# Optimization experiments

Measured on AMD Instinct MI355X. Metric: run time of the kernel, lower is better.

## Reference

```python
import jax, jax.numpy as jnp
import numpy as np

B, IN, P, H, OUT = 131072, 40, 128, 256, 1

def setup_inputs() -> dict:
    key = jax.random.key(0)
    ks = jax.random.split(key, 10)
    s_in, s_h = 1.0 / np.sqrt(IN), 1.0 / np.sqrt(H)
    return {
        "x_step": jax.random.normal(ks[0], (B, 1, IN), jnp.float32),
        "hidden_in": jax.random.normal(ks[1], (1, B, H), jnp.float32),
        "W_proj": jax.random.uniform(ks[2], (P, IN), jnp.float32, -s_in, s_in),
        "b_proj": jax.random.uniform(ks[3], (P,), jnp.float32, -s_in, s_in),
        "W_ih": jax.random.uniform(ks[4], (3 * H, P), jnp.float32, -s_h, s_h),
        "W_hh": jax.random.uniform(ks[5], (3 * H, H), jnp.float32, -s_h, s_h),
        "b_ih": jax.random.uniform(ks[6], (3 * H,), jnp.float32, -s_h, s_h),
        "b_hh": jax.random.uniform(ks[7], (3 * H,), jnp.float32, -s_h, s_h),
        "W_head": jax.random.uniform(ks[8], (OUT, H), jnp.float32, -s_h, s_h),
        "b_head": jax.random.uniform(ks[9], (OUT,), jnp.float32, -s_h, s_h),
    }

def reference(x_step, hidden_in, W_proj, b_proj, W_ih, W_hh, b_ih, b_hh, W_head, b_head):
    # input projection: [B,1,IN] -> [B,P]
    x = jnp.einsum('bi,pi->bp', x_step[:, 0, :], W_proj) + b_proj
    h = hidden_in[0]  # [B,H]
    # single GRU step (PyTorch gate layout: reset, update, new)
    gi = jnp.einsum('bp,gp->bg', x, W_ih) + b_ih  # [B,3H]
    gh = jnp.einsum('bh,gh->bg', h, W_hh) + b_hh  # [B,3H]
    i_r, i_z, i_n = jnp.split(gi, 3, axis=-1)
    h_r, h_z, h_n = jnp.split(gh, 3, axis=-1)
    r = jax.nn.sigmoid(i_r + h_r)
    z = jax.nn.sigmoid(i_z + h_z)
    n = jnp.tanh(i_n + r * h_n)
    h_new = (1.0 - z) * n + z * h  # [B,H]
    pred = jnp.einsum('bh,oh->bo', h_new, W_head) + b_head  # [B,OUT]
    return pred[:, None, :], h_new[None]  # ([B,1,OUT], [1,B,H])
```

## Files before the change

### kernel.cpp

```cpp
#include <hip/hip_runtime.h>

#define B_N 131072
#define IN_N 40
#define H_N 256

typedef __bf16 bf16x8 __attribute__((ext_vector_type(8)));
typedef float f32x4 __attribute__((ext_vector_type(4)));

#define MFMA(a, b, c) __builtin_amdgcn_mfma_f32_16x16x32_bf16(a, b, c, 0, 0, 0)

#define WSQ 61440
#define WSBI (4 * WSQ)
#define PREP_N (245760 + 768 + B_N)

__global__ void prep(const float* __restrict__ Wp, const float* __restrict__ bp,
                     const float* __restrict__ Wih, const float* __restrict__ Whh,
                     const float* __restrict__ bih, const float* __restrict__ bhead,
                     __bf16* __restrict__ wsb, float* __restrict__ out) {
  int i = blockIdx.x * 256 + threadIdx.x;
  if (i < WSBI) {
    const int quarter = i / WSQ, r = i % WSQ;
    if (r < 49152) {
      const int g = r >> 14, ks = (r >> 11) & 7, sub = (r >> 9) & 3,
                col = (r >> 3) & 63, e = r & 7;
      const int gatecol = g * 256 + quarter * 64 + col;
      const int k = ks * 32 + sub * 8 + e;
      wsb[i] = (__bf16)Whh[(size_t)gatecol * 256 + k];
    } else {
      const int rr = r - 49152;
      const int g = rr >> 12, ks = (rr >> 11) & 1, sub = (rr >> 9) & 3,
                col = (rr >> 3) & 63, e = rr & 7;
      const int gatecol = g * 256 + quarter * 64 + col;
      const int k = ks * 32 + sub * 8 + e;
      float v = 0.f;
      if (k < IN_N)
        for (int p = 0; p < 128; ++p)
          v += Wih[(size_t)gatecol * 128 + p] * Wp[p * IN_N + k];
      wsb[i] = (__bf16)v;
    }
  } else if (i < WSBI + 768) {
    const int g = i - WSBI;
    float v = bih[g];
    for (int p = 0; p < 128; ++p) v += Wih[g * 128 + p] * bp[p];
    ((float*)(wsb + WSBI))[g] = v;
  } else if (i < PREP_N) {
    out[i - (WSBI + 768)] = bhead[0];
  }
}

__device__ __forceinline__ void gload16(const __bf16* g, __bf16* l) {
  __builtin_amdgcn_global_load_lds(
      (const __attribute__((address_space(1))) void*)g,
      (__attribute__((address_space(3))) void*)l, 16, 0, 0);
}

__device__ __forceinline__ bf16x8 cvt8(float4 a, float4 b) {
  bf16x8 u;
  u[0] = (__bf16)a.x; u[1] = (__bf16)a.y; u[2] = (__bf16)a.z; u[3] = (__bf16)a.w;
  u[4] = (__bf16)b.x; u[5] = (__bf16)b.y; u[6] = (__bf16)b.z; u[7] = (__bf16)b.w;
  return u;
}

__global__ __launch_bounds__(512, 1) void gru_v13(
    const float* __restrict__ x, const float* __restrict__ h0,
    const __bf16* __restrict__ wsb, const float* __restrict__ bhh,
    const float* __restrict__ Whead, float* __restrict__ out) {
  __shared__ __bf16 Wl[WSQ];
  __shared__ __bf16 hsw[16384];
  __shared__ __bf16 xsw[4096];

  const int tid = threadIdx.x;
  const int lane = tid & 63;
  const int w = tid >> 6;
  const int l15 = lane & 15;
  const int l4 = lane >> 4;
  const int rw = w >> 2, cw = w & 3;

  const int lin = (blockIdx.x & 7) * 128 + (blockIdx.x >> 3);
  const int quarter = lin & 3;
  const int rgrp = lin >> 2;
  const size_t row0 = (size_t)rgrp * 512;

  const int colB = cw * 16 + l15;
  const int hcol = quarter * 64 + colB;

  const __bf16* wsq = wsb + quarter * WSQ;
#pragma unroll
  for (int j = 0; j < 15; ++j) {
    const int c = (w * 15 + j) * 512;
    gload16(wsq + c + lane * 8, &Wl[c]);
  }

  if (tid < 192) {
    const int row = tid / 3, cz = 5 + tid % 3;
    bf16x8 z = {};
    *reinterpret_cast<bf16x8*>(&xsw[row * 64 + ((cz ^ (row & 7)) << 3)]) = z;
  }

  const float* bfused = (const float*)(wsb + WSBI);
  const float bR = bfused[hcol] + bhh[hcol];
  const float bZ = bfused[256 + hcol] + bhh[256 + hcol];
  const float bI = bfused[512 + hcol];
  const float bH = bhh[512 + hcol];
  const float wh = Whead[hcol];

  float4 shv[8], sxv[2];
  const int xrow = tid / 5, xci = tid % 5;
  auto issueStage = [&](int t) {
    const float* hb = h0 + (row0 + (size_t)t * 64) * H_N;
#pragma unroll
    for (int j = 0; j < 4; ++j) {
      const int g = tid + j * 512;
      shv[2 * j]     = *reinterpret_cast<const float4*>(hb + g * 8);
      shv[2 * j + 1] = *reinterpret_cast<const float4*>(hb + g * 8 + 4);
    }
    if (tid < 320) {
      const float* xb = x + (row0 + (size_t)t * 64) * IN_N + xrow * IN_N + xci * 8;
      sxv[0] = *reinterpret_cast<const float4*>(xb);
      sxv[1] = *reinterpret_cast<const float4*>(xb + 4);
    }
  };
  auto writeStage = [&]() {
#pragma unroll
    for (int j = 0; j < 4; ++j) {
      const int g = tid + j * 512;
      const int row = g >> 5, ci = g & 31;
      *reinterpret_cast<bf16x8*>(&hsw[row * 256 + ((ci ^ (row & 7)) << 3)]) =
          cvt8(shv[2 * j], shv[2 * j + 1]);
    }
    if (tid < 320)
      *reinterpret_cast<bf16x8*>(&xsw[xrow * 64 + ((xci ^ (xrow & 7)) << 3)]) =
          cvt8(sxv[0], sxv[1]);
  };

  issueStage(0);
  writeStage();
  __syncthreads();

  for (int t = 0; t < 8; ++t) {
    if (t < 7) issueStage(t + 1);

    f32x4 aR[2], aZ[2], aI[2], aH[2];
#pragma unroll
    for (int mi = 0; mi < 2; ++mi) {
      aR[mi] = (f32x4){bR, bR, bR, bR};
      aZ[mi] = (f32x4){bZ, bZ, bZ, bZ};
      aI[mi] = (f32x4){bI, bI, bI, bI};
      aH[mi] = (f32x4){bH, bH, bH, bH};
    }

#pragma unroll
    for (int ks = 0; ks < 10; ++ks) {
      bf16x8 b0, b1, b2;
      if (ks < 2) {
        const int base = 49152 + l4 * 512 + colB * 8;
        b0 = *reinterpret_cast<const bf16x8*>(&Wl[base + (0 * 2 + ks) * 2048]);
        b1 = *reinterpret_cast<const bf16x8*>(&Wl[base + (1 * 2 + ks) * 2048]);
        b2 = *reinterpret_cast<const bf16x8*>(&Wl[base + (2 * 2 + ks) * 2048]);
      } else {
        const int base = l4 * 512 + colB * 8;
        b0 = *reinterpret_cast<const bf16x8*>(&Wl[base + (0 * 8 + ks - 2) * 2048]);
        b1 = *reinterpret_cast<const bf16x8*>(&Wl[base + (1 * 8 + ks - 2) * 2048]);
        b2 = *reinterpret_cast<const bf16x8*>(&Wl[base + (2 * 8 + ks - 2) * 2048]);
      }
#pragma unroll
      for (int mi = 0; mi < 2; ++mi) {
        const int row = rw * 32 + mi * 16 + l15;
        bf16x8 a;
        if (ks < 2)
          a = *reinterpret_cast<const bf16x8*>(
              &xsw[row * 64 + (((ks * 4 + l4) ^ (row & 7)) << 3)]);
        else
          a = *reinterpret_cast<const bf16x8*>(
              &hsw[row * 256 + ((((ks - 2) * 4 + l4) ^ (row & 7)) << 3)]);
        aR[mi] = MFMA(a, b0, aR[mi]);
        aZ[mi] = MFMA(a, b1, aZ[mi]);
        if (ks < 2) aI[mi] = MFMA(a, b2, aI[mi]);
        else        aH[mi] = MFMA(a, b2, aH[mi]);
      }
    }

    const size_t trow = row0 + (size_t)t * 64;
    const int chc = quarter * 8 + (colB >> 3), cofs = colB & 7;
    float ps[2][4];
#pragma unroll
    for (int mi = 0; mi < 2; ++mi) {
#pragma unroll
      for (int r = 0; r < 4; ++r) {
        const int rowl = rw * 32 + mi * 16 + l4 * 4 + r;
        const float rg = 1.f / (1.f + __expf(-aR[mi][r]));
        const float zg = 1.f / (1.f + __expf(-aZ[mi][r]));
        const float e2 = __expf(2.f * (aI[mi][r] + rg * aH[mi][r]));
        const float ng = (e2 - 1.f) / (e2 + 1.f);
        const float hv = (float)hsw[rowl * 256 + ((chc ^ (rowl & 7)) << 3) + cofs];
        const float hn = (1.f - zg) * ng + zg * hv;
        out[(size_t)B_N + (trow + rowl) * H_N + hcol] = hn;
        ps[mi][r] = hn * wh;
      }
    }
#pragma unroll
    for (int mi = 0; mi < 2; ++mi)
#pragma unroll
      for (int r = 0; r < 4; ++r) {
        float s = ps[mi][r];
        s += __shfl_xor(s, 1);
        s += __shfl_xor(s, 2);
        s += __shfl_xor(s, 4);
        s += __shfl_xor(s, 8);
        if (l15 == 0)
          atomicAdd(&out[trow + rw * 32 + mi * 16 + l4 * 4 + r], s);
      }

    __syncthreads();
    if (t < 7) {
      writeStage();
      __syncthreads();
    }
  }
}

extern "C" void kernel_launch(void* const* d_in, const int* in_sizes, int n_in,
                              void* d_out, int out_size, void* d_ws, size_t ws_size,
                              hipStream_t stream) {
  const float* x     = (const float*)d_in[0];
  const float* h0    = (const float*)d_in[1];
  const float* Wp    = (const float*)d_in[2];
  const float* bp    = (const float*)d_in[3];
  const float* Wih   = (const float*)d_in[4];
  const float* Whh   = (const float*)d_in[5];
  const float* bih   = (const float*)d_in[6];
  const float* bhh   = (const float*)d_in[7];
  const float* Whead = (const float*)d_in[8];
  const float* bhead = (const float*)d_in[9];
  float* out = (float*)d_out;
  __bf16* wsb = (__bf16*)d_ws;

  prep<<<(PREP_N + 255) / 256, 256, 0, stream>>>(Wp, bp, Wih, Whh, bih, bhead, wsb, out);
  gru_v13<<<1024, 512, 0, stream>>>(x, h0, wsb, bhh, Whead, out);
}
```

Baseline: 194.9 us.

## Double waves per block, shrink per-wave row tile, overlap stage write with epilogue

The workgroup grows from 512 to 1024 threads. Each of the 16 waves now computes one 16-row MFMA tile instead of two, and the staging loads and weight-to-LDS loads are spread across the larger block. The next h/x stage is written into LDS right after the MFMA loop, behind a single barrier, so one barrier per step is removed. The epilogue reads the previous hidden value from global fp32 instead of from the bf16 LDS copy. The aim is more waves to hide latency and fewer syncs, at the cost of halved B-fragment reuse per wave (more LDS reads) and extra global reads of h0.

After: 179.5 us. 1.09x faster.

```diff
diff --git a/kernel.cpp b/kernel.cpp
--- a/kernel.cpp
+++ b/kernel.cpp
@@ -61,7 +61,7 @@
   return u;
 }
 
-__global__ __launch_bounds__(512, 1) void gru_v13(
+__global__ __launch_bounds__(1024, 1) void gru_v14(
     const float* __restrict__ x, const float* __restrict__ h0,
     const __bf16* __restrict__ wsb, const float* __restrict__ bhh,
     const float* __restrict__ Whead, float* __restrict__ out) {
@@ -86,9 +86,10 @@
 
   const __bf16* wsq = wsb + quarter * WSQ;
 #pragma unroll
-  for (int j = 0; j < 15; ++j) {
-    const int c = (w * 15 + j) * 512;
-    gload16(wsq + c + lane * 8, &Wl[c]);
+  for (int j = 0; j < 8; ++j) {
+    const int idx = j * 16 + w;
+    if (idx < 120)
+      gload16(wsq + idx * 512 + lane * 8, &Wl[idx * 512]);
   }
 
   if (tid < 192) {
@@ -104,13 +105,13 @@
   const float bH = bhh[512 + hcol];
   const float wh = Whead[hcol];
 
-  float4 shv[8], sxv[2];
+  float4 shv[4], sxv[2];
   const int xrow = tid / 5, xci = tid % 5;
   auto issueStage = [&](int t) {
     const float* hb = h0 + (row0 + (size_t)t * 64) * H_N;
 #pragma unroll
-    for (int j = 0; j < 4; ++j) {
-      const int g = tid + j * 512;
+    for (int j = 0; j < 2; ++j) {
+      const int g = tid + j * 1024;
       shv[2 * j]     = *reinterpret_cast<const float4*>(hb + g * 8);
       shv[2 * j + 1] = *reinterpret_cast<const float4*>(hb + g * 8 + 4);
     }
@@ -122,8 +123,8 @@
   };
   auto writeStage = [&]() {
 #pragma unroll
-    for (int j = 0; j < 4; ++j) {
-      const int g = tid + j * 512;
+    for (int j = 0; j < 2; ++j) {
+      const int g = tid + j * 1024;
       const int row = g >> 5, ci = g & 31;
       *reinterpret_cast<bf16x8*>(&hsw[row * 256 + ((ci ^ (row & 7)) << 3)]) =
           cvt8(shv[2 * j], shv[2 * j + 1]);
@@ -140,82 +141,66 @@
   for (int t = 0; t < 8; ++t) {
     if (t < 7) issueStage(t + 1);
 
-    f32x4 aR[2], aZ[2], aI[2], aH[2];
-#pragma unroll
-    for (int mi = 0; mi < 2; ++mi) {
-      aR[mi] = (f32x4){bR, bR, bR, bR};
-      aZ[mi] = (f32x4){bZ, bZ, bZ, bZ};
-      aI[mi] = (f32x4){bI, bI, bI, bI};
-      aH[mi] = (f32x4){bH, bH, bH, bH};
-    }
-
+    f32x4 aR = {bR, bR, bR, bR};
+    f32x4 aZ = {bZ, bZ, bZ, bZ};
+    f32x4 aI = {bI, bI, bI, bI};
+    f32x4 aH = {bH, bH, bH, bH};
+
+    const int arow = rw * 16 + l15;
 #pragma unroll
     for (int ks = 0; ks < 10; ++ks) {
-      bf16x8 b0, b1, b2;
+      bf16x8 b0, b1, b2, a;
       if (ks < 2) {
         const int base = 49152 + l4 * 512 + colB * 8;
         b0 = *reinterpret_cast<const bf16x8*>(&Wl[base + (0 * 2 + ks) * 2048]);
         b1 = *reinterpret_cast<const bf16x8*>(&Wl[base + (1 * 2 + ks) * 2048]);
         b2 = *reinterpret_cast<const bf16x8*>(&Wl[base + (2 * 2 + ks) * 2048]);
+        a = *reinterpret_cast<const bf16x8*>(
+            &xsw[arow * 64 + (((ks * 4 + l4) ^ (arow & 7)) << 3)]);
       } else {
         const int base = l4 * 512 + colB * 8;
         b0 = *reinterpret_cast<const bf16x8*>(&Wl[base + (0 * 8 + ks - 2) * 2048]);
         b1 = *reinterpret_cast<const bf16x8*>(&Wl[base + (1 * 8 + ks - 2) * 2048]);
         b2 = *reinterpret_cast<const bf16x8*>(&Wl[base + (2 * 8 + ks - 2) * 2048]);
+        a = *reinterpret_cast<const bf16x8*>(
+            &hsw[arow * 256 + ((((ks - 2) * 4 + l4) ^ (arow & 7)) << 3)]);
       }
-#pragma unroll
-      for (int mi = 0; mi < 2; ++mi) {
-        const int row = rw * 32 + mi * 16 + l15;
-        bf16x8 a;
-        if (ks < 2)
-          a = *reinterpret_cast<const bf16x8*>(
-              &xsw[row * 64 + (((ks * 4 + l4) ^ (row & 7)) << 3)]);
-        else
-          a = *reinterpret_cast<const bf16x8*>(
-              &hsw[row * 256 + ((((ks - 2) * 4 + l4) ^ (row & 7)) << 3)]);
-        aR[mi] = MFMA(a, b0, aR[mi]);
-        aZ[mi] = MFMA(a, b1, aZ[mi]);
-        if (ks < 2) aI[mi] = MFMA(a, b2, aI[mi]);
-        else        aH[mi] = MFMA(a, b2, aH[mi]);
-      }
-    }
+      aR = MFMA(a, b0, aR);
+      aZ = MFMA(a, b1, aZ);
+      if (ks < 2) aI = MFMA(a, b2, aI);
+      else        aH = MFMA(a, b2, aH);
+    }
+
+    __syncthreads();
+
+    if (t < 7) writeStage();
 
     const size_t trow = row0 + (size_t)t * 64;
-    const int chc = quarter * 8 + (colB >> 3), cofs = colB & 7;
-    float ps[2][4];
-#pragma unroll
-    for (int mi = 0; mi < 2; ++mi) {
-#pragma unroll
-      for (int r = 0; r < 4; ++r) {
-        const int rowl = rw * 32 + mi * 16 + l4 * 4 + r;
-        const float rg = 1.f / (1.f + __expf(-aR[mi][r]));
-        const float zg = 1.f / (1.f + __expf(-aZ[mi][r]));
-        const float e2 = __expf(2.f * (aI[mi][r] + rg * aH[mi][r]));
-        const float ng = (e2 - 1.f) / (e2 + 1.f);
-        const float hv = (float)hsw[rowl * 256 + ((chc ^ (rowl & 7)) << 3) + cofs];
-        const float hn = (1.f - zg) * ng + zg * hv;
-        out[(size_t)B_N + (trow + rowl) * H_N + hcol] = hn;
-        ps[mi][r] = hn * wh;
-      }
-    }
-#pragma unroll
-    for (int mi = 0; mi < 2; ++mi)
-#pragma unroll
-      for (int r = 0; r < 4; ++r) {
-        float s = ps[mi][r];
-        s += __shfl_xor(s, 1);
-        s += __shfl_xor(s, 2);
-        s += __shfl_xor(s, 4);
-        s += __shfl_xor(s, 8);
-        if (l15 == 0)
-          atomicAdd(&out[trow + rw * 32 + mi * 16 + l4 * 4 + r], s);
-      }
-
-    __syncthreads();
-    if (t < 7) {
-      writeStage();
-      __syncthreads();
-    }
+    float ps[4];
+#pragma unroll
+    for (int r = 0; r < 4; ++r) {
+      const int rowl = rw * 16 + l4 * 4 + r;
+      const float rg = 1.f / (1.f + __expf(-aR[r]));
+      const float zg = 1.f / (1.f + __expf(-aZ[r]));
+      const float e2 = __expf(2.f * (aI[r] + rg * aH[r]));
+      const float ng = (e2 - 1.f) / (e2 + 1.f);
+      const float hv = h0[(trow + rowl) * H_N + hcol];
+      const float hn = (1.f - zg) * ng + zg * hv;
+      out[(size_t)B_N + (trow + rowl) * H_N + hcol] = hn;
+      ps[r] = hn * wh;
+    }
+#pragma unroll
+    for (int r = 0; r < 4; ++r) {
+      float s = ps[r];
+      s += __shfl_xor(s, 1);
+      s += __shfl_xor(s, 2);
+      s += __shfl_xor(s, 4);
+      s += __shfl_xor(s, 8);
+      if (l15 == 0)
+        atomicAdd(&out[trow + rw * 16 + l4 * 4 + r], s);
+    }
+
+    if (t < 7) __syncthreads();
   }
 }
 
@@ -236,5 +221,5 @@
   __bf16* wsb = (__bf16*)d_ws;
 
   prep<<<(PREP_N + 255) / 256, 256, 0, stream>>>(Wp, bp, Wih, Whh, bih, bhead, wsb, out);
-  gru_v13<<<1024, 512, 0, stream>>>(x, h0, wsb, bhh, Whead, out);
-}
+  gru_v14<<<1024, 1024, 0, stream>>>(x, h0, wsb, bhh, Whead, out);
+}
```

## Replace persistent 8-tile loop with one 128-row tile per 1024-thread block

Applied to the files above, without the earlier changes.

Replaces the persistent blocks, which each looped over eight 64-row tiles with register-staged prefetch, with 4096 blocks of 1024 threads that each handle one 128-row tile. The x-projection and hidden weight slices now share one LDS buffer that is reused across phases. The intent is more parallelism and less per-block serialization, with load latency hidden by many resident waves instead of explicit software pipelining. In exchange, every block reloads its weight slice into LDS (four times as many weight loads overall), extra barriers are added, and h is re-read from global memory in fp32 for the blend.

Result: slower. 271.8 us (+39.4%).

```diff
diff --git a/kernel.cpp b/kernel.cpp
--- a/kernel.cpp
+++ b/kernel.cpp
@@ -61,13 +61,12 @@
   return u;
 }
 
-__global__ __launch_bounds__(512, 1) void gru_v13(
+__global__ __launch_bounds__(1024, 1) void gru_v16(
     const float* __restrict__ x, const float* __restrict__ h0,
     const __bf16* __restrict__ wsb, const float* __restrict__ bhh,
     const float* __restrict__ Whead, float* __restrict__ out) {
-  __shared__ __bf16 Wl[WSQ];
-  __shared__ __bf16 hsw[16384];
-  __shared__ __bf16 xsw[4096];
+  __shared__ __bf16 WG[49152];
+  __shared__ __bf16 AH[32768];
 
   const int tid = threadIdx.x;
   const int lane = tid & 63;
@@ -76,25 +75,46 @@
   const int l4 = lane >> 4;
   const int rw = w >> 2, cw = w & 3;
 
-  const int lin = (blockIdx.x & 7) * 128 + (blockIdx.x >> 3);
+  const int lin = (blockIdx.x & 7) * 512 + (blockIdx.x >> 3);
   const int quarter = lin & 3;
-  const int rgrp = lin >> 2;
-  const size_t row0 = (size_t)rgrp * 512;
+  const size_t row0 = (size_t)(lin >> 2) * 128;
 
   const int colB = cw * 16 + l15;
   const int hcol = quarter * 64 + colB;
 
   const __bf16* wsq = wsb + quarter * WSQ;
 #pragma unroll
-  for (int j = 0; j < 15; ++j) {
-    const int c = (w * 15 + j) * 512;
-    gload16(wsq + c + lane * 8, &Wl[c]);
-  }
-
-  if (tid < 192) {
-    const int row = tid / 3, cz = 5 + tid % 3;
+  for (int j = 0; j < 6; ++j) {
+    const int idx = w * 6 + j;
+    gload16(wsq + idx * 512 + lane * 8, &WG[idx * 512]);
+  }
+#pragma unroll
+  for (int j = 0; j < 2; ++j) {
+    const int idx = j * 16 + w;
+    if (idx < 24)
+      gload16(wsq + 49152 + idx * 512 + lane * 8, &AH[idx * 512]);
+  }
+
+  bf16x8 hreg[4];
+#pragma unroll
+  for (int j = 0; j < 4; ++j) {
+    const int c = tid + j * 1024;
+    const float* s = h0 + (row0 + (c >> 5)) * H_N + (c & 31) * 8;
+    hreg[j] = cvt8(*reinterpret_cast<const float4*>(s),
+                   *reinterpret_cast<const float4*>(s + 4));
+  }
+
+  if (tid < 640) {
+    const int row = tid / 5, kc = tid % 5;
+    const float* s = x + (row0 + row) * IN_N + kc * 8;
+    *reinterpret_cast<bf16x8*>(&AH[12288 + row * 64 + ((kc ^ (row & 7)) << 3)]) =
+        cvt8(*reinterpret_cast<const float4*>(s),
+             *reinterpret_cast<const float4*>(s + 4));
+  } else {
+    const int p = tid - 640;
+    const int row = p / 3, kc = 5 + p % 3;
     bf16x8 z = {};
-    *reinterpret_cast<bf16x8*>(&xsw[row * 64 + ((cz ^ (row & 7)) << 3)]) = z;
+    *reinterpret_cast<bf16x8*>(&AH[12288 + row * 64 + ((kc ^ (row & 7)) << 3)]) = z;
   }
 
   const float* bfused = (const float*)(wsb + WSBI);
@@ -104,119 +124,86 @@
   const float bH = bhh[512 + hcol];
   const float wh = Whead[hcol];
 
-  float4 shv[8], sxv[2];
-  const int xrow = tid / 5, xci = tid % 5;
-  auto issueStage = [&](int t) {
-    const float* hb = h0 + (row0 + (size_t)t * 64) * H_N;
-#pragma unroll
-    for (int j = 0; j < 4; ++j) {
-      const int g = tid + j * 512;
-      shv[2 * j]     = *reinterpret_cast<const float4*>(hb + g * 8);
-      shv[2 * j + 1] = *reinterpret_cast<const float4*>(hb + g * 8 + 4);
-    }
-    if (tid < 320) {
-      const float* xb = x + (row0 + (size_t)t * 64) * IN_N + xrow * IN_N + xci * 8;
-      sxv[0] = *reinterpret_cast<const float4*>(xb);
-      sxv[1] = *reinterpret_cast<const float4*>(xb + 4);
-    }
-  };
-  auto writeStage = [&]() {
-#pragma unroll
-    for (int j = 0; j < 4; ++j) {
-      const int g = tid + j * 512;
-      const int row = g >> 5, ci = g & 31;
-      *reinterpret_cast<bf16x8*>(&hsw[row * 256 + ((ci ^ (row & 7)) << 3)]) =
-          cvt8(shv[2 * j], shv[2 * j + 1]);
-    }
-    if (tid < 320)
-      *reinterpret_cast<bf16x8*>(&xsw[xrow * 64 + ((xci ^ (xrow & 7)) << 3)]) =
-          cvt8(sxv[0], sxv[1]);
-  };
-
-  issueStage(0);
-  writeStage();
   __syncthreads();
 
-  for (int t = 0; t < 8; ++t) {
-    if (t < 7) issueStage(t + 1);
-
-    f32x4 aR[2], aZ[2], aI[2], aH[2];
+  f32x4 aR[2], aZ[2], aI[2], aH4[2];
+#pragma unroll
+  for (int mi = 0; mi < 2; ++mi) {
+    aR[mi] = (f32x4){bR, bR, bR, bR};
+    aZ[mi] = (f32x4){bZ, bZ, bZ, bZ};
+    aI[mi] = (f32x4){bI, bI, bI, bI};
+    aH4[mi] = (f32x4){bH, bH, bH, bH};
+  }
+  const int bofs = l4 * 512 + colB * 8;
+#pragma unroll
+  for (int ks = 0; ks < 2; ++ks) {
+    const bf16x8 b0 = *reinterpret_cast<const bf16x8*>(&AH[(0 + ks) * 2048 + bofs]);
+    const bf16x8 b1 = *reinterpret_cast<const bf16x8*>(&AH[(2 + ks) * 2048 + bofs]);
+    const bf16x8 b2 = *reinterpret_cast<const bf16x8*>(&AH[(4 + ks) * 2048 + bofs]);
 #pragma unroll
     for (int mi = 0; mi < 2; ++mi) {
-      aR[mi] = (f32x4){bR, bR, bR, bR};
-      aZ[mi] = (f32x4){bZ, bZ, bZ, bZ};
-      aI[mi] = (f32x4){bI, bI, bI, bI};
-      aH[mi] = (f32x4){bH, bH, bH, bH};
-    }
-
-#pragma unroll
-    for (int ks = 0; ks < 10; ++ks) {
-      bf16x8 b0, b1, b2;
-      if (ks < 2) {
-        const int base = 49152 + l4 * 512 + colB * 8;
-        b0 = *reinterpret_cast<const bf16x8*>(&Wl[base + (0 * 2 + ks) * 2048]);
-        b1 = *reinterpret_cast<const bf16x8*>(&Wl[base + (1 * 2 + ks) * 2048]);
-        b2 = *reinterpret_cast<const bf16x8*>(&Wl[base + (2 * 2 + ks) * 2048]);
-      } else {
-        const int base = l4 * 512 + colB * 8;
-        b0 = *reinterpret_cast<const bf16x8*>(&Wl[base + (0 * 8 + ks - 2) * 2048]);
-        b1 = *reinterpret_cast<const bf16x8*>(&Wl[base + (1 * 8 + ks - 2) * 2048]);
-        b2 = *reinterpret_cast<const bf16x8*>(&Wl[base + (2 * 8 + ks - 2) * 2048]);
-      }
-#pragma unroll
-      for (int mi = 0; mi < 2; ++mi) {
-        const int row = rw * 32 + mi * 16 + l15;
-        bf16x8 a;
-        if (ks < 2)
-          a = *reinterpret_cast<const bf16x8*>(
-              &xsw[row * 64 + (((ks * 4 + l4) ^ (row & 7)) << 3)]);
-        else
-          a = *reinterpret_cast<const bf16x8*>(
-              &hsw[row * 256 + ((((ks - 2) * 4 + l4) ^ (row & 7)) << 3)]);
-        aR[mi] = MFMA(a, b0, aR[mi]);
-        aZ[mi] = MFMA(a, b1, aZ[mi]);
-        if (ks < 2) aI[mi] = MFMA(a, b2, aI[mi]);
-        else        aH[mi] = MFMA(a, b2, aH[mi]);
-      }
-    }
-
-    const size_t trow = row0 + (size_t)t * 64;
-    const int chc = quarter * 8 + (colB >> 3), cofs = colB & 7;
-    float ps[2][4];
+      const int arow = rw * 32 + mi * 16 + l15;
+      const bf16x8 a = *reinterpret_cast<const bf16x8*>(
+          &AH[12288 + arow * 64 + (((ks * 4 + l4) ^ (arow & 7)) << 3)]);
+      aR[mi] = MFMA(a, b0, aR[mi]);
+      aZ[mi] = MFMA(a, b1, aZ[mi]);
+      aI[mi] = MFMA(a, b2, aI[mi]);
+    }
+  }
+  __syncthreads();
+
+#pragma unroll
+  for (int j = 0; j < 4; ++j) {
+    const int c = tid + j * 1024;
+    const int row = c >> 5, ci = c & 31;
+    *reinterpret_cast<bf16x8*>(&AH[row * 256 + ((ci ^ (row & 7)) << 3)]) = hreg[j];
+  }
+  __syncthreads();
+
+#pragma unroll
+  for (int ks = 0; ks < 8; ++ks) {
+    const bf16x8 b0 = *reinterpret_cast<const bf16x8*>(&WG[(0 + ks) * 2048 + bofs]);
+    const bf16x8 b1 = *reinterpret_cast<const bf16x8*>(&WG[(8 + ks) * 2048 + bofs]);
+    const bf16x8 b2 = *reinterpret_cast<const bf16x8*>(&WG[(16 + ks) * 2048 + bofs]);
 #pragma unroll
     for (int mi = 0; mi < 2; ++mi) {
-#pragma unroll
-      for (int r = 0; r < 4; ++r) {
-        const int rowl = rw * 32 + mi * 16 + l4 * 4 + r;
-        const float rg = 1.f / (1.f + __expf(-aR[mi][r]));
-        const float zg = 1.f / (1.f + __expf(-aZ[mi][r]));
-        const float e2 = __expf(2.f * (aI[mi][r] + rg * aH[mi][r]));
-        const float ng = (e2 - 1.f) / (e2 + 1.f);
-        const float hv = (float)hsw[rowl * 256 + ((chc ^ (rowl & 7)) << 3) + cofs];
-        const float hn = (1.f - zg) * ng + zg * hv;
-        out[(size_t)B_N + (trow + rowl) * H_N + hcol] = hn;
-        ps[mi][r] = hn * wh;
-      }
-    }
-#pragma unroll
-    for (int mi = 0; mi < 2; ++mi)
-#pragma unroll
-      for (int r = 0; r < 4; ++r) {
-        float s = ps[mi][r];
-        s += __shfl_xor(s, 1);
-        s += __shfl_xor(s, 2);
-        s += __shfl_xor(s, 4);
-        s += __shfl_xor(s, 8);
-        if (l15 == 0)
-          atomicAdd(&out[trow + rw * 32 + mi * 16 + l4 * 4 + r], s);
-      }
-
-    __syncthreads();
-    if (t < 7) {
-      writeStage();
-      __syncthreads();
-    }
-  }
+      const int arow = rw * 32 + mi * 16 + l15;
+      const bf16x8 a = *reinterpret_cast<const bf16x8*>(
+          &AH[arow * 256 + (((ks * 4 + l4) ^ (arow & 7)) << 3)]);
+      aR[mi] = MFMA(a, b0, aR[mi]);
+      aZ[mi] = MFMA(a, b1, aZ[mi]);
+      aH4[mi] = MFMA(a, b2, aH4[mi]);
+    }
+  }
+
+  float ps[2][4];
+#pragma unroll
+  for (int mi = 0; mi < 2; ++mi) {
+#pragma unroll
+    for (int r = 0; r < 4; ++r) {
+      const int rowl = rw * 32 + mi * 16 + l4 * 4 + r;
+      const float rg = 1.f / (1.f + __expf(-aR[mi][r]));
+      const float zg = 1.f / (1.f + __expf(-aZ[mi][r]));
+      const float e2 = __expf(2.f * (aI[mi][r] + rg * aH4[mi][r]));
+      const float ng = (e2 - 1.f) / (e2 + 1.f);
+      const float hv = h0[(row0 + rowl) * H_N + hcol];
+      const float hn = (1.f - zg) * ng + zg * hv;
+      out[(size_t)B_N + (row0 + rowl) * H_N + hcol] = hn;
+      ps[mi][r] = hn * wh;
+    }
+  }
+#pragma unroll
+  for (int mi = 0; mi < 2; ++mi)
+#pragma unroll
+    for (int r = 0; r < 4; ++r) {
+      float s = ps[mi][r];
+      s += __shfl_xor(s, 1);
+      s += __shfl_xor(s, 2);
+      s += __shfl_xor(s, 4);
+      s += __shfl_xor(s, 8);
+      if (l15 == 0)
+        atomicAdd(&out[row0 + rw * 32 + mi * 16 + l4 * 4 + r], s);
+    }
 }
 
 extern "C" void kernel_launch(void* const* d_in, const int* in_sizes, int n_in,
@@ -236,5 +223,5 @@
   __bf16* wsb = (__bf16*)d_ws;
 
   prep<<<(PREP_N + 255) / 256, 256, 0, stream>>>(Wp, bp, Wih, Whh, bih, bhead, wsb, out);
-  gru_v13<<<1024, 512, 0, stream>>>(x, h0, wsb, bhh, Whead, out);
-}
+  gru_v16<<<4096, 1024, 0, stream>>>(x, h0, wsb, bhh, Whead, out);
+}
```
